# Kernel tuning notes

Hardware: AMD Instinct MI355X
Metric: run time of the kernel (lower is better)

The kernel has to match this reference:

```python
import jax, jax.numpy as jnp
import numpy as np

VOCAB = 32000
EMB = 300
DEC_UNITS = 512
UNITS = 2 * DEC_UNITS        # GRU units = 1024
ENC_DIM = 1024               # encoder output feature dim
B, S = 256, 128
IN_DIM = ENC_DIM + EMB       # GRU input: [context ; embedding] = 1324


def setup_inputs() -> dict:
    key = jax.random.key(0)
    ks = jax.random.split(key, 16)
    sc = 0.02
    return {
        "x": jax.random.randint(ks[0], (B, 1), 0, VOCAB),
        "state": jax.random.normal(ks[1], (B, UNITS), jnp.float32),
        "encoder_output": jax.random.normal(ks[2], (B, S, ENC_DIM), jnp.float32),
        "emb": jax.random.normal(ks[3], (VOCAB, EMB), jnp.float32) * sc,
        "W1": jax.random.normal(ks[4], (ENC_DIM, DEC_UNITS), jnp.float32) * sc,
        "b1": jnp.zeros((DEC_UNITS,), jnp.float32),
        "W2": jax.random.normal(ks[5], (UNITS, DEC_UNITS), jnp.float32) * sc,
        "b2": jnp.zeros((DEC_UNITS,), jnp.float32),
        "V": jax.random.normal(ks[6], (DEC_UNITS, 1), jnp.float32) * sc,
        "bV": jnp.zeros((1,), jnp.float32),
        "gru_k": jax.random.normal(ks[7], (IN_DIM, 3 * UNITS), jnp.float32) * sc,
        "gru_rk": jax.random.normal(ks[8], (UNITS, 3 * UNITS), jnp.float32) * sc,
        "gru_b": jnp.zeros((2, 3 * UNITS), jnp.float32),  # [input_bias, recurrent_bias] (reset_after=True)
        "fc_W": jax.random.normal(ks[9], (UNITS, VOCAB), jnp.float32) * sc,
        "fc_b": jnp.zeros((VOCAB,), jnp.float32),
    }


def reference(x, state, encoder_output, emb, W1, b1, W2, b2, V, bV,
              gru_k, gru_rk, gru_b, fc_W, fc_b):
    # --- Bahdanau attention (query = state, values = encoder_output) ---
    # score: [B, S, 1]
    q = state @ W2 + b2                                    # [B, U_att]
    score = jnp.tanh(encoder_output @ W1 + b1 + q[:, None, :]) @ V + bV
    attn = jax.nn.softmax(score, axis=1)                   # [B, S, 1]
    context = jnp.sum(attn * encoder_output, axis=1)       # [B, ENC_DIM]

    # --- embed token and concat with context (seq len 1) ---
    x_emb = emb[x[:, 0]]                                   # [B, EMB]
    xi = jnp.concatenate([context, x_emb], axis=-1)        # [B, IN_DIM]

    # --- single GRU step (Keras GRU, reset_after=True, inference: no dropout) ---
    mx = xi @ gru_k + gru_b[0]                             # [B, 3U]
    mh = state @ gru_rk + gru_b[1]                         # [B, 3U]
    xz, xr, xh = jnp.split(mx, 3, axis=-1)
    hz, hr, hh_rec = jnp.split(mh, 3, axis=-1)
    z = jax.nn.sigmoid(xz + hz)
    r = jax.nn.sigmoid(xr + hr)
    hh = jnp.tanh(xh + r * hh_rec)
    h = z * state + (1.0 - z) * hh                         # [B, UNITS]

    # --- softmax projection over vocab ---
    probs = jax.nn.softmax(h @ fc_W + fc_b, axis=-1)       # [B, VOCAB]
    return probs, h, attn
```

## Files before the change

kernel.cpp:

```cpp
#include <hip/hip_runtime.h>
#include <math.h>

#define B_    256
#define S_    128
#define ENCD  1024
#define DECU  512
#define UNITS 1024
#define VOCAB 32000
#define EMB_  300
#define INDIM 1324
#define KPADX 1344
#define G3    3072

typedef __bf16 bf16x8 __attribute__((ext_vector_type(8)));
typedef __bf16 bf16x4 __attribute__((ext_vector_type(4)));
typedef __bf16 bf16x2 __attribute__((ext_vector_type(2)));
typedef float  f32x4  __attribute__((ext_vector_type(4)));

#define MFMA16(a, b, c) __builtin_amdgcn_mfma_f32_16x16x32_bf16((a), (b), (c), 0, 0, 0)

__device__ __forceinline__ int swz(int row, int e) { return row * 64 + (e ^ ((row & 7) << 3)); }

__device__ __forceinline__ void gl_lds16(const void* g, void* l) {
  __builtin_amdgcn_global_load_lds((const __attribute__((address_space(1))) void*)g,
                                   (__attribute__((address_space(3))) void*)l, 16, 0, 0);
}

__device__ __forceinline__ float fast_tanh(float x) {
  x = fminf(fmaxf(x, -15.f), 15.f);
  float e = __expf(2.f * x);
  return (e - 1.f) / (e + 1.f);
}

__global__ __launch_bounds__(256) void k_prep(const float* __restrict__ enc,
                                              __bf16* __restrict__ enc_bf,
                                              const float* __restrict__ state,
                                              __bf16* __restrict__ state_bf) {
  int bid = blockIdx.x;
  if (bid < 4096) {
    for (int g = bid * 256 + threadIdx.x; g < (B_ * S_ * ENCD) / 8; g += 4096 * 256) {
      const float* p = enc + (size_t)g * 8;
      float4 f0 = *(const float4*)p;
      float4 f1 = *(const float4*)(p + 4);
      bf16x8 o = {(__bf16)f0.x, (__bf16)f0.y, (__bf16)f0.z, (__bf16)f0.w,
                  (__bf16)f1.x, (__bf16)f1.y, (__bf16)f1.z, (__bf16)f1.w};
      *(bf16x8*)(enc_bf + (size_t)g * 8) = o;
    }
  } else {
    int i4 = (bid - 4096) * 256 + threadIdx.x;
    float4 f = *(const float4*)(state + (size_t)i4 * 4);
    bf16x4 o = {(__bf16)f.x, (__bf16)f.y, (__bf16)f.z, (__bf16)f.w};
    *(bf16x4*)(state_bf + (size_t)i4 * 4) = o;
  }
}

__global__ __launch_bounds__(1024) void k_w1t(const float* __restrict__ W1,
                                              __bf16* __restrict__ W1t) {
  int n = blockIdx.x;
  int k = threadIdx.x;
  W1t[(size_t)n * 1024 + k] = (__bf16)W1[(size_t)k * 512 + n];
}

template <int BM>
__global__ __launch_bounds__(512) void k_gemm2(const __bf16* __restrict__ A, int ldaK,
                                               const float* __restrict__ B,
                                               const float* __restrict__ bias,
                                               float* __restrict__ C, int K, int N) {
  constexpr int WR = (BM == 64) ? 2 : 4;
  constexpr int WN = 8 / WR;
  constexpr int MI = BM / (WR * 16);
  constexpr int NI = 64 / (WN * 16);
  __shared__ __align__(16) __bf16 As[2][BM * 64];
  __shared__ __align__(16) __bf16 Bs[2][64 * 64];
  int tid = threadIdx.x, lane = tid & 63, w = tid >> 6;
  int wr = w / WN, wn = w % WN;
  int m0 = blockIdx.x * BM, n0 = blockIdx.y * 64;
  int lrow = lane & 15, lk = (lane >> 4) * 8;
  int r0 = wr * MI * 16, c0 = wn * NI * 16;
  f32x4 acc[MI][NI] = {};

  constexpr int ACH = BM / 64;
  constexpr int TPR = 8 / ACH;
  bf16x8 pfa[ACH];
  float pfb[8];
  int am = tid / TPR, aks = (tid % TPR) * (ACH * 8);
  const __bf16* arow = A + (size_t)(m0 + am) * ldaK + aks;
  int bn = tid & 63, bks = (tid >> 6) * 8;
  int nk = (K + 63) >> 6;

#pragma unroll
  for (int c = 0; c < ACH; ++c) pfa[c] = *(const bf16x8*)(arow + c * 8);
#pragma unroll
  for (int i = 0; i < 8; ++i) { int k = bks + i; pfb[i] = (k < K) ? B[(size_t)k * N + n0 + bn] : 0.f; }
#pragma unroll
  for (int c = 0; c < ACH; ++c) *(bf16x8*)&As[0][swz(am, aks + c * 8)] = pfa[c];
  {
    __bf16 tb[8];
#pragma unroll
    for (int i = 0; i < 8; ++i) tb[i] = (__bf16)pfb[i];
    *(bf16x8*)&Bs[0][swz(bn, bks)] = *(bf16x8*)&tb[0];
  }
  __syncthreads();

  int cur = 0;
  for (int it = 0; it < nk; ++it) {
    bool more = (it + 1 < nk);
    if (more) {
      int k0 = (it + 1) * 64;
#pragma unroll
      for (int c = 0; c < ACH; ++c) pfa[c] = *(const bf16x8*)(arow + k0 + c * 8);
#pragma unroll
      for (int i = 0; i < 8; ++i) { int k = k0 + bks + i; pfb[i] = (k < K) ? B[(size_t)k * N + n0 + bn] : 0.f; }
    }
    const __bf16* Ac = As[cur];
    const __bf16* Bc = Bs[cur];
#pragma unroll
    for (int kk = 0; kk < 64; kk += 32) {
      bf16x8 av[MI], bv[NI];
#pragma unroll
      for (int mi = 0; mi < MI; ++mi) { int r = r0 + mi * 16 + lrow; av[mi] = *(const bf16x8*)&Ac[swz(r, kk + lk)]; }
#pragma unroll
      for (int ni = 0; ni < NI; ++ni) { int r = c0 + ni * 16 + lrow; bv[ni] = *(const bf16x8*)&Bc[swz(r, kk + lk)]; }
#pragma unroll
      for (int mi = 0; mi < MI; ++mi)
#pragma unroll
        for (int ni = 0; ni < NI; ++ni) acc[mi][ni] = MFMA16(av[mi], bv[ni], acc[mi][ni]);
    }
    if (more) {
#pragma unroll
      for (int c = 0; c < ACH; ++c) *(bf16x8*)&As[cur ^ 1][swz(am, aks + c * 8)] = pfa[c];
      __bf16 tb[8];
#pragma unroll
      for (int i = 0; i < 8; ++i) tb[i] = (__bf16)pfb[i];
      *(bf16x8*)&Bs[cur ^ 1][swz(bn, bks)] = *(bf16x8*)&tb[0];
      __syncthreads();
      cur ^= 1;
    }
  }
#pragma unroll
  for (int mi = 0; mi < MI; ++mi)
#pragma unroll
    for (int ni = 0; ni < NI; ++ni) {
      int colg = n0 + c0 + ni * 16 + lrow;
      float bvv = bias[colg];
#pragma unroll
      for (int reg = 0; reg < 4; ++reg) {
        int rowg = m0 + r0 + mi * 16 + (lane >> 4) * 4 + reg;
        C[(size_t)rowg * N + colg] = acc[mi][ni][reg] + bvv;
      }
    }
}

__global__ __launch_bounds__(256) void k_score7(const __bf16* __restrict__ enc_bf,
                                                const __bf16* __restrict__ W1t,
                                                const float* __restrict__ b1,
                                                const float* __restrict__ q,
                                                const float* __restrict__ V,
                                                float* __restrict__ sc_part) {
  __shared__ __align__(16) __bf16 As[2][128 * 64];
  __shared__ __align__(16) __bf16 Bs[2][128 * 64];
  __shared__ float red[2][128];
  int b = blockIdx.x, by = blockIdx.y;
  int m0 = b * 128, n0 = by * 128;
  int tid = threadIdx.x, lane = tid & 63, w = tid >> 6;
  int wr = w >> 1, wn = w & 1;
  int lrow = lane & 15, lk = (lane >> 4) * 8;
  int r0 = wr * 64, c0 = wn * 64;
  f32x4 acc[4][4] = {};

  int srow = lane >> 3;
  int sslot = (lane & 7) ^ (srow & 7);
  const __bf16* asrc[4];
  const __bf16* bsrc[4];
#pragma unroll
  for (int c = 0; c < 4; ++c) {
    int row = (w * 4 + c) * 8 + srow;
    asrc[c] = enc_bf + (size_t)(m0 + row) * 1024 + sslot * 8;
    bsrc[c] = W1t + (size_t)(n0 + row) * 1024 + sslot * 8;
  }

#pragma unroll
  for (int c = 0; c < 4; ++c) gl_lds16(asrc[c], &As[0][(w * 4 + c) * 512]);
#pragma unroll
  for (int c = 0; c < 4; ++c) gl_lds16(bsrc[c], &Bs[0][(w * 4 + c) * 512]);
  __syncthreads();

  int cur = 0;
  for (int it = 0; it < 16; ++it) {
    bool more = (it + 1 < 16);
    if (more) {
      int k0 = (it + 1) * 64;
#pragma unroll
      for (int c = 0; c < 4; ++c) gl_lds16(asrc[c] + k0, &As[cur ^ 1][(w * 4 + c) * 512]);
#pragma unroll
      for (int c = 0; c < 4; ++c) gl_lds16(bsrc[c] + k0, &Bs[cur ^ 1][(w * 4 + c) * 512]);
    }
    const __bf16* Ac = As[cur];
    const __bf16* Bc = Bs[cur];
#pragma unroll
    for (int kk = 0; kk < 64; kk += 32) {
      bf16x8 av[4], bv[4];
#pragma unroll
      for (int mi = 0; mi < 4; ++mi) { int r = r0 + mi * 16 + lrow; av[mi] = *(const bf16x8*)&Ac[swz(r, kk + lk)]; }
#pragma unroll
      for (int ni = 0; ni < 4; ++ni) { int r = c0 + ni * 16 + lrow; bv[ni] = *(const bf16x8*)&Bc[swz(r, kk + lk)]; }
#pragma unroll
      for (int mi = 0; mi < 4; ++mi)
#pragma unroll
        for (int ni = 0; ni < 4; ++ni) acc[mi][ni] = MFMA16(av[mi], bv[ni], acc[mi][ni]);
    }
    if (more) {
      __syncthreads();
      cur ^= 1;
    }
  }
  float psum[4][4] = {};
#pragma unroll
  for (int mi = 0; mi < 4; ++mi)
#pragma unroll
    for (int ni = 0; ni < 4; ++ni) {
      int j = n0 + c0 + ni * 16 + lrow;
      float vj = V[j], b1j = b1[j], qv = q[(size_t)b * DECU + j];
#pragma unroll
      for (int reg = 0; reg < 4; ++reg)
        psum[mi][reg] += vj * fast_tanh(acc[mi][ni][reg] + b1j + qv);
    }
#pragma unroll
  for (int off = 1; off < 16; off <<= 1)
#pragma unroll
    for (int mi = 0; mi < 4; ++mi)
#pragma unroll
      for (int reg = 0; reg < 4; ++reg)
        psum[mi][reg] += __shfl_xor(psum[mi][reg], off);
  __syncthreads();
  if (lrow == 0) {
#pragma unroll
    for (int mi = 0; mi < 4; ++mi)
#pragma unroll
      for (int reg = 0; reg < 4; ++reg)
        red[wn][r0 + mi * 16 + (lane >> 4) * 4 + reg] = psum[mi][reg];
  }
  __syncthreads();
  if (tid < 128)
    sc_part[((size_t)b * 128 + tid) * 4 + by] = red[0][tid] + red[1][tid];
}

__global__ __launch_bounds__(256) void k_ctx4(const float* __restrict__ sc_part,
                                              const float* __restrict__ bV,
                                              const __bf16* __restrict__ enc_bf,
                                              const int* __restrict__ x,
                                              const float* __restrict__ emb,
                                              float* __restrict__ attn_out,
                                              __bf16* __restrict__ xi_bf) {
  int b = blockIdx.x, chunk = blockIdx.y, t = threadIdx.x;
  int lane = t & 63, w = t >> 6;
  __shared__ float a_s[S_];
  __shared__ float part[4][128];
  if (t < S_) {
    float4 p = *(const float4*)&sc_part[((size_t)b * 128 + t) * 4];
    a_s[t] = bV[0] + p.x + p.y + p.z + p.w;
  }
  __syncthreads();
  float mx = -INFINITY;
  for (int s = 0; s < S_; ++s) mx = fmaxf(mx, a_s[s]);
  float sum = 0.f;
  for (int s = 0; s < S_; ++s) sum += __expf(a_s[s] - mx);
  float inv = 1.f / sum;
  __syncthreads();
  if (t < S_) {
    float av = __expf(a_s[t] - mx) * inv;
    a_s[t] = av;
    if (chunk == 0) attn_out[(size_t)b * S_ + t] = av;
  }
  __syncthreads();
  int c0 = chunk * 128;
  float a0 = 0.f, a1 = 0.f;
  const __bf16* eb = enc_bf + ((size_t)b * S_ + w * 32) * ENCD + c0 + lane * 2;
#pragma unroll 8
  for (int s = 0; s < 32; ++s) {
    bf16x2 e = *(const bf16x2*)(eb + (size_t)s * ENCD);
    float av = a_s[w * 32 + s];
    a0 = fmaf(av, (float)e[0], a0);
    a1 = fmaf(av, (float)e[1], a1);
  }
  part[w][lane * 2 + 0] = a0;
  part[w][lane * 2 + 1] = a1;
  __syncthreads();
  if (t < 128) {
    float v = part[0][t] + part[1][t] + part[2][t] + part[3][t];
    xi_bf[(size_t)b * KPADX + c0 + t] = (__bf16)v;
  }
  if (chunk == 0) {
    int xb = x[b];
    if (t < 75) {
      float4 f = *(const float4*)&emb[(size_t)xb * EMB_ + t * 4];
      bf16x4 o4 = {(__bf16)f.x, (__bf16)f.y, (__bf16)f.z, (__bf16)f.w};
      *(bf16x4*)&xi_bf[(size_t)b * KPADX + ENCD + t * 4] = o4;
    } else if (t < 80) {
      bf16x4 z = {(__bf16)0.f, (__bf16)0.f, (__bf16)0.f, (__bf16)0.f};
      *(bf16x4*)&xi_bf[(size_t)b * KPADX + INDIM + (t - 75) * 4] = z;
    }
  }
}

__global__ __launch_bounds__(256) void k_gates(const float* __restrict__ mx,
                                               const float* __restrict__ mh,
                                               const float* __restrict__ state,
                                               float* __restrict__ h_out,
                                               __bf16* __restrict__ h_bf) {
  int idx = blockIdx.x * 256 + threadIdx.x;
  int b = idx >> 10, j = idx & 1023;
  const float* mxr = mx + (size_t)b * G3;
  const float* mhr = mh + (size_t)b * G3;
  float z = 1.f / (1.f + __expf(-(mxr[j] + mhr[j])));
  float r = 1.f / (1.f + __expf(-(mxr[UNITS + j] + mhr[UNITS + j])));
  float hh = tanhf(mxr[2 * UNITS + j] + r * mhr[2 * UNITS + j]);
  float st = state[idx];
  float h = z * st + (1.f - z) * hh;
  h_out[idx] = h;
  h_bf[idx] = (__bf16)h;
}

__global__ __launch_bounds__(1024) void k_softmax(float* __restrict__ logits) {
  int b = blockIdx.x, t = threadIdx.x;
  int lane = t & 63, w = t >> 6;
  float4* row4 = (float4*)(logits + (size_t)b * VOCAB);
  __shared__ float redm[16];
  __shared__ float reds[16];
  float4 v[8];
  float m = -INFINITY;
#pragma unroll
  for (int i = 0; i < 8; ++i) {
    int i4 = i * 1024 + t;
    if (i4 < 8000) {
      v[i] = row4[i4];
      m = fmaxf(m, fmaxf(fmaxf(v[i].x, v[i].y), fmaxf(v[i].z, v[i].w)));
    } else {
      v[i] = make_float4(-INFINITY, -INFINITY, -INFINITY, -INFINITY);
    }
  }
#pragma unroll
  for (int o = 32; o >= 1; o >>= 1) m = fmaxf(m, __shfl_xor(m, o));
  if (lane == 0) redm[w] = m;
  __syncthreads();
  float m2 = -INFINITY;
#pragma unroll
  for (int i = 0; i < 16; ++i) m2 = fmaxf(m2, redm[i]);
  float s = 0.f;
#pragma unroll
  for (int i = 0; i < 8; ++i) {
    v[i].x = __expf(v[i].x - m2);
    v[i].y = __expf(v[i].y - m2);
    v[i].z = __expf(v[i].z - m2);
    v[i].w = __expf(v[i].w - m2);
    s += v[i].x + v[i].y + v[i].z + v[i].w;
  }
#pragma unroll
  for (int o = 32; o >= 1; o >>= 1) s += __shfl_xor(s, o);
  if (lane == 0) reds[w] = s;
  __syncthreads();
  float s2 = 0.f;
#pragma unroll
  for (int i = 0; i < 16; ++i) s2 += reds[i];
  float inv = 1.f / s2;
#pragma unroll
  for (int i = 0; i < 8; ++i) {
    int i4 = i * 1024 + t;
    if (i4 < 8000)
      row4[i4] = make_float4(v[i].x * inv, v[i].y * inv, v[i].z * inv, v[i].w * inv);
  }
}

extern "C" void kernel_launch(void* const* d_in, const int* in_sizes, int n_in,
                              void* d_out, int out_size, void* d_ws, size_t ws_size,
                              hipStream_t stream) {
  const int*   x     = (const int*)d_in[0];
  const float* state = (const float*)d_in[1];
  const float* enc   = (const float*)d_in[2];
  const float* emb   = (const float*)d_in[3];
  const float* W1    = (const float*)d_in[4];
  const float* b1    = (const float*)d_in[5];
  const float* W2    = (const float*)d_in[6];
  const float* b2    = (const float*)d_in[7];
  const float* V     = (const float*)d_in[8];
  const float* bV    = (const float*)d_in[9];
  const float* gru_k = (const float*)d_in[10];
  const float* gru_rk= (const float*)d_in[11];
  const float* gru_b = (const float*)d_in[12];
  const float* fc_W  = (const float*)d_in[13];
  const float* fc_b  = (const float*)d_in[14];

  float* out   = (float*)d_out;
  float* probs = out;
  float* h_out = out + (size_t)B_ * VOCAB;
  float* attn  = h_out + (size_t)B_ * UNITS;

  char* wsb = (char*)d_ws;
  const size_t ENC_BF_BYTES = (size_t)B_ * S_ * ENCD * 2;
  __bf16* enc_bf  = (__bf16*)wsb;
  __bf16* W1t     = (__bf16*)(wsb + ENC_BF_BYTES);
  __bf16* state_bf= (__bf16*)(wsb + ENC_BF_BYTES + 1048576);
  __bf16* xi_bf   = (__bf16*)(wsb + ENC_BF_BYTES + 1572864);
  __bf16* h_bf    = (__bf16*)(wsb + ENC_BF_BYTES + 2260992);
  float*  q       = (float*)(wsb + ENC_BF_BYTES + 2785280);
  float*  sc_part = (float*)(wsb + ENC_BF_BYTES + 3309568);
  float*  mx      = (float*)(wsb + ENC_BF_BYTES + 3833856);
  float*  mh      = (float*)(wsb + ENC_BF_BYTES + 6979584);

  k_prep<<<4352, 256, 0, stream>>>(enc, enc_bf, state, state_bf);
  k_w1t<<<512, 1024, 0, stream>>>(W1, W1t);
  k_gemm2<64><<<dim3(4, 8), 512, 0, stream>>>(state_bf, UNITS, W2, b2, q, UNITS, DECU);
  k_score7<<<dim3(B_, 4), 256, 0, stream>>>(enc_bf, W1t, b1, q, V, sc_part);
  k_ctx4<<<dim3(B_, 8), 256, 0, stream>>>(sc_part, bV, enc_bf, x, emb, attn, xi_bf);
  k_gemm2<64><<<dim3(4, 48), 512, 0, stream>>>(xi_bf, KPADX, gru_k, gru_b, mx, INDIM, G3);
  k_gemm2<64><<<dim3(4, 48), 512, 0, stream>>>(state_bf, UNITS, gru_rk, gru_b + G3, mh, UNITS, G3);
  k_gates<<<(B_ * UNITS) / 256, 256, 0, stream>>>(mx, mh, state, h_out, h_bf);
  k_gemm2<256><<<dim3(1, VOCAB / 64), 512, 0, stream>>>(h_bf, UNITS, fc_W, fc_b, probs, UNITS, VOCAB);
  k_softmax<<<B_, 1024, 0, stream>>>(probs);
}
```

Baseline: 242.5 us.

## Merge state GEMMs into one launch and triple-buffer score kernel loads

Both GEMMs that read state (W2 for the attention query and gru_rk for the recurrent gates) now run in a single launch, with the grid split along N between the two output buffers. This drops a kernel launch and gives the small q GEMM more parallel blocks. The score kernel moves to 512 threads with a three-stage LDS ring buffer and explicit vmcnt waits, keeping two tiles in flight, and it hoists the V/b1/q epilogue loads. The cost is more LDS per block, which may lower occupancy, and hand-tuned waitcnt logic that must stay in step with the load count.

```diff
diff --git a/kernel.cpp b/kernel.cpp
--- a/kernel.cpp
+++ b/kernel.cpp
@@ -151,91 +151,192 @@
     }
 }
 
-__global__ __launch_bounds__(256) void k_score7(const __bf16* __restrict__ enc_bf,
+__global__ __launch_bounds__(512) void k_gemm2d(const __bf16* __restrict__ A, int ldaK,
+                                                const float* __restrict__ B1,
+                                                const float* __restrict__ bias1,
+                                                float* __restrict__ C1, int N1,
+                                                const float* __restrict__ B2,
+                                                const float* __restrict__ bias2,
+                                                float* __restrict__ C2, int N2,
+                                                int K) {
+  constexpr int BM = 64, MI = 2, NI = 1;
+  __shared__ __align__(16) __bf16 As[2][BM * 64];
+  __shared__ __align__(16) __bf16 Bs[2][64 * 64];
+  int tid = threadIdx.x, lane = tid & 63, w = tid >> 6;
+  int wr = w >> 2, wn = w & 3;
+  int m0 = blockIdx.x * BM;
+  int n0 = blockIdx.y * 64;
+  const float* B; const float* bias; float* C; int N;
+  if (n0 < N1) { B = B1; bias = bias1; C = C1; N = N1; }
+  else         { B = B2; bias = bias2; C = C2; N = N2; n0 -= N1; }
+  int lrow = lane & 15, lk = (lane >> 4) * 8;
+  int r0 = wr * MI * 16, c0 = wn * NI * 16;
+  f32x4 acc[MI][NI] = {};
+
+  bf16x8 pfa;
+  float pfb[8];
+  int am = tid >> 3, aks = (tid & 7) * 8;
+  const __bf16* arow = A + (size_t)(m0 + am) * ldaK + aks;
+  int bn = tid & 63, bks = (tid >> 6) * 8;
+  int nk = (K + 63) >> 6;
+
+  pfa = *(const bf16x8*)(arow);
+#pragma unroll
+  for (int i = 0; i < 8; ++i) { int k = bks + i; pfb[i] = (k < K) ? B[(size_t)k * N + n0 + bn] : 0.f; }
+  *(bf16x8*)&As[0][swz(am, aks)] = pfa;
+  {
+    __bf16 tb[8];
+#pragma unroll
+    for (int i = 0; i < 8; ++i) tb[i] = (__bf16)pfb[i];
+    *(bf16x8*)&Bs[0][swz(bn, bks)] = *(bf16x8*)&tb[0];
+  }
+  __syncthreads();
+
+  int cur = 0;
+  for (int it = 0; it < nk; ++it) {
+    bool more = (it + 1 < nk);
+    if (more) {
+      int k0 = (it + 1) * 64;
+      pfa = *(const bf16x8*)(arow + k0);
+#pragma unroll
+      for (int i = 0; i < 8; ++i) { int k = k0 + bks + i; pfb[i] = (k < K) ? B[(size_t)k * N + n0 + bn] : 0.f; }
+    }
+    const __bf16* Ac = As[cur];
+    const __bf16* Bc = Bs[cur];
+#pragma unroll
+    for (int kk = 0; kk < 64; kk += 32) {
+      bf16x8 av[MI], bv[NI];
+#pragma unroll
+      for (int mi = 0; mi < MI; ++mi) { int r = r0 + mi * 16 + lrow; av[mi] = *(const bf16x8*)&Ac[swz(r, kk + lk)]; }
+#pragma unroll
+      for (int ni = 0; ni < NI; ++ni) { int r = c0 + ni * 16 + lrow; bv[ni] = *(const bf16x8*)&Bc[swz(r, kk + lk)]; }
+#pragma unroll
+      for (int mi = 0; mi < MI; ++mi)
+#pragma unroll
+        for (int ni = 0; ni < NI; ++ni) acc[mi][ni] = MFMA16(av[mi], bv[ni], acc[mi][ni]);
+    }
+    if (more) {
+      *(bf16x8*)&As[cur ^ 1][swz(am, aks)] = pfa;
+      __bf16 tb[8];
+#pragma unroll
+      for (int i = 0; i < 8; ++i) tb[i] = (__bf16)pfb[i];
+      *(bf16x8*)&Bs[cur ^ 1][swz(bn, bks)] = *(bf16x8*)&tb[0];
+      __syncthreads();
+      cur ^= 1;
+    }
+  }
+#pragma unroll
+  for (int mi = 0; mi < MI; ++mi)
+#pragma unroll
+    for (int ni = 0; ni < NI; ++ni) {
+      int colg = n0 + c0 + ni * 16 + lrow;
+      float bvv = bias[colg];
+#pragma unroll
+      for (int reg = 0; reg < 4; ++reg) {
+        int rowg = m0 + r0 + mi * 16 + (lane >> 4) * 4 + reg;
+        C[(size_t)rowg * N + colg] = acc[mi][ni][reg] + bvv;
+      }
+    }
+}
+
+__global__ __launch_bounds__(512) void k_score8(const __bf16* __restrict__ enc_bf,
                                                 const __bf16* __restrict__ W1t,
                                                 const float* __restrict__ b1,
                                                 const float* __restrict__ q,
                                                 const float* __restrict__ V,
                                                 float* __restrict__ sc_part) {
-  __shared__ __align__(16) __bf16 As[2][128 * 64];
-  __shared__ __align__(16) __bf16 Bs[2][128 * 64];
+  __shared__ __align__(16) __bf16 As[3][128 * 64];
+  __shared__ __align__(16) __bf16 Bs[3][128 * 64];
   __shared__ float red[2][128];
   int b = blockIdx.x, by = blockIdx.y;
   int m0 = b * 128, n0 = by * 128;
   int tid = threadIdx.x, lane = tid & 63, w = tid >> 6;
   int wr = w >> 1, wn = w & 1;
   int lrow = lane & 15, lk = (lane >> 4) * 8;
-  int r0 = wr * 64, c0 = wn * 64;
-  f32x4 acc[4][4] = {};
-
+  int r0 = wr * 32, c0 = wn * 64;
+  f32x4 acc[2][4] = {};
+
+  float vj[4], b1j[4], qv[4];
+#pragma unroll
+  for (int ni = 0; ni < 4; ++ni) {
+    int j = n0 + c0 + ni * 16 + lrow;
+    vj[ni] = V[j]; b1j[ni] = b1[j]; qv[ni] = q[(size_t)b * DECU + j];
+  }
   int srow = lane >> 3;
   int sslot = (lane & 7) ^ (srow & 7);
-  const __bf16* asrc[4];
-  const __bf16* bsrc[4];
-#pragma unroll
-  for (int c = 0; c < 4; ++c) {
-    int row = (w * 4 + c) * 8 + srow;
+  const __bf16* asrc[2];
+  const __bf16* bsrc[2];
+  int ch0 = w * 2;
+#pragma unroll
+  for (int c = 0; c < 2; ++c) {
+    int row = (ch0 + c) * 8 + srow;
     asrc[c] = enc_bf + (size_t)(m0 + row) * 1024 + sslot * 8;
     bsrc[c] = W1t + (size_t)(n0 + row) * 1024 + sslot * 8;
   }
-
-#pragma unroll
-  for (int c = 0; c < 4; ++c) gl_lds16(asrc[c], &As[0][(w * 4 + c) * 512]);
-#pragma unroll
-  for (int c = 0; c < 4; ++c) gl_lds16(bsrc[c], &Bs[0][(w * 4 + c) * 512]);
-  __syncthreads();
-
-  int cur = 0;
+  asm volatile("s_waitcnt vmcnt(0)" ::: "memory");
+
+#pragma unroll
+  for (int t = 0; t < 2; ++t) {
+    int k0 = t * 64;
+#pragma unroll
+    for (int c = 0; c < 2; ++c) {
+      gl_lds16(asrc[c] + k0, &As[t][(ch0 + c) * 512]);
+      gl_lds16(bsrc[c] + k0, &Bs[t][(ch0 + c) * 512]);
+    }
+  }
+  asm volatile("s_waitcnt vmcnt(4)" ::: "memory");
+  __builtin_amdgcn_s_barrier();
+
+#pragma unroll
   for (int it = 0; it < 16; ++it) {
-    bool more = (it + 1 < 16);
-    if (more) {
-      int k0 = (it + 1) * 64;
-#pragma unroll
-      for (int c = 0; c < 4; ++c) gl_lds16(asrc[c] + k0, &As[cur ^ 1][(w * 4 + c) * 512]);
-#pragma unroll
-      for (int c = 0; c < 4; ++c) gl_lds16(bsrc[c] + k0, &Bs[cur ^ 1][(w * 4 + c) * 512]);
-    }
-    const __bf16* Ac = As[cur];
-    const __bf16* Bc = Bs[cur];
+    if (it + 2 < 16) {
+      int k0 = (it + 2) * 64, bi = (it + 2) % 3;
+#pragma unroll
+      for (int c = 0; c < 2; ++c) {
+        gl_lds16(asrc[c] + k0, &As[bi][(ch0 + c) * 512]);
+        gl_lds16(bsrc[c] + k0, &Bs[bi][(ch0 + c) * 512]);
+      }
+    }
+    const __bf16* Ac = As[it % 3];
+    const __bf16* Bc = Bs[it % 3];
 #pragma unroll
     for (int kk = 0; kk < 64; kk += 32) {
-      bf16x8 av[4], bv[4];
-#pragma unroll
-      for (int mi = 0; mi < 4; ++mi) { int r = r0 + mi * 16 + lrow; av[mi] = *(const bf16x8*)&Ac[swz(r, kk + lk)]; }
+      bf16x8 av[2], bv[4];
+#pragma unroll
+      for (int mi = 0; mi < 2; ++mi) { int r = r0 + mi * 16 + lrow; av[mi] = *(const bf16x8*)&Ac[swz(r, kk + lk)]; }
 #pragma unroll
       for (int ni = 0; ni < 4; ++ni) { int r = c0 + ni * 16 + lrow; bv[ni] = *(const bf16x8*)&Bc[swz(r, kk + lk)]; }
 #pragma unroll
-      for (int mi = 0; mi < 4; ++mi)
+      for (int mi = 0; mi < 2; ++mi)
 #pragma unroll
         for (int ni = 0; ni < 4; ++ni) acc[mi][ni] = MFMA16(av[mi], bv[ni], acc[mi][ni]);
     }
-    if (more) {
-      __syncthreads();
-      cur ^= 1;
-    }
-  }
-  float psum[4][4] = {};
-#pragma unroll
-  for (int mi = 0; mi < 4; ++mi)
+    if (it < 15) {
+      if (it < 14) asm volatile("s_waitcnt vmcnt(4)" ::: "memory");
+      else         asm volatile("s_waitcnt vmcnt(0)" ::: "memory");
+      __builtin_amdgcn_s_barrier();
+    }
+  }
+  float psum[2][4] = {};
+#pragma unroll
+  for (int mi = 0; mi < 2; ++mi)
 #pragma unroll
     for (int ni = 0; ni < 4; ++ni) {
-      int j = n0 + c0 + ni * 16 + lrow;
-      float vj = V[j], b1j = b1[j], qv = q[(size_t)b * DECU + j];
 #pragma unroll
       for (int reg = 0; reg < 4; ++reg)
-        psum[mi][reg] += vj * fast_tanh(acc[mi][ni][reg] + b1j + qv);
+        psum[mi][reg] += vj[ni] * fast_tanh(acc[mi][ni][reg] + b1j[ni] + qv[ni]);
     }
 #pragma unroll
   for (int off = 1; off < 16; off <<= 1)
 #pragma unroll
-    for (int mi = 0; mi < 4; ++mi)
+    for (int mi = 0; mi < 2; ++mi)
 #pragma unroll
       for (int reg = 0; reg < 4; ++reg)
         psum[mi][reg] += __shfl_xor(psum[mi][reg], off);
   __syncthreads();
   if (lrow == 0) {
 #pragma unroll
-    for (int mi = 0; mi < 4; ++mi)
+    for (int mi = 0; mi < 2; ++mi)
 #pragma unroll
       for (int reg = 0; reg < 4; ++reg)
         red[wn][r0 + mi * 16 + (lane >> 4) * 4 + reg] = psum[mi][reg];
@@ -409,11 +510,12 @@
 
   k_prep<<<4352, 256, 0, stream>>>(enc, enc_bf, state, state_bf);
   k_w1t<<<512, 1024, 0, stream>>>(W1, W1t);
-  k_gemm2<64><<<dim3(4, 8), 512, 0, stream>>>(state_bf, UNITS, W2, b2, q, UNITS, DECU);
-  k_score7<<<dim3(B_, 4), 256, 0, stream>>>(enc_bf, W1t, b1, q, V, sc_part);
+  k_gemm2d<<<dim3(4, 56), 512, 0, stream>>>(state_bf, UNITS,
+                                            gru_rk, gru_b + G3, mh, G3,
+                                            W2, b2, q, DECU, UNITS);
+  k_score8<<<dim3(B_, 4), 512, 0, stream>>>(enc_bf, W1t, b1, q, V, sc_part);
   k_ctx4<<<dim3(B_, 8), 256, 0, stream>>>(sc_part, bV, enc_bf, x, emb, attn, xi_bf);
   k_gemm2<64><<<dim3(4, 48), 512, 0, stream>>>(xi_bf, KPADX, gru_k, gru_b, mx, INDIM, G3);
-  k_gemm2<64><<<dim3(4, 48), 512, 0, stream>>>(state_bf, UNITS, gru_rk, gru_b + G3, mh, UNITS, G3);
   k_gates<<<(B_ * UNITS) / 256, 256, 0, stream>>>(mx, mh, state, h_out, h_bf);
   k_gemm2<256><<<dim3(1, VOCAB / 64), 512, 0, stream>>>(h_bf, UNITS, fc_W, fc_b, probs, UNITS, VOCAB);
   k_softmax<<<B_, 1024, 0, stream>>>(probs);
```

Result: faster. 231.7 us (-4.4%).
